# Kernel tuning notes

Measured on AMD Instinct MI355X. Metric: run time of the kernel, lower is better.

## Reference

```python
import jax, jax.numpy as jnp
import numpy as np

B, IN, H = 4096, 1024, 1024
G = 5  # i, f, o, c_hat, s gates

def setup_inputs() -> dict:
    key = jax.random.key(0)
    ks = jax.random.split(key, 24)
    s_in = 1.0 / np.sqrt(IN)
    s_h = 1.0 / np.sqrt(H)
    s_cat = 1.0 / np.sqrt(IN + H)
    inp = {
        'x': jax.random.normal(ks[0], (B, IN), jnp.float32),
        'h_prev': jax.random.normal(ks[1], (B, H), jnp.float32),
        'c_prev': jax.random.normal(ks[2], (B, H), jnp.float32),
        'ssg_state': jax.random.normal(ks[3], (B, H), jnp.float32),
        # stacked gate weights, torch Linear convention y = x @ W.T + b
        'Wx': jax.random.uniform(ks[4], (G, H, IN), jnp.float32, -s_in, s_in),
        'bWx': jax.random.uniform(ks[5], (G, H), jnp.float32, -s_in, s_in),
        'Ux': jax.random.uniform(ks[6], (G, H, H), jnp.float32, -s_h, s_h),
        'bUx': jax.random.uniform(ks[7], (G, H), jnp.float32, -s_h, s_h),
        # alpha MLP: Linear(IN+H -> H), ReLU, Linear(H -> 1), Sigmoid
        'a1_w': jax.random.uniform(ks[8], (H, IN + H), jnp.float32, -s_cat, s_cat),
        'a1_b': jax.random.uniform(ks[9], (H,), jnp.float32, -s_cat, s_cat),
        'a2_w': jax.random.uniform(ks[10], (1, H), jnp.float32, -s_h, s_h),
        'a2_b': jax.random.uniform(ks[11], (1,), jnp.float32, -s_h, s_h),
        'r1_w': jax.random.uniform(ks[12], (H, H), jnp.float32, -s_h, s_h),
        'r1_b': jax.random.uniform(ks[13], (H,), jnp.float32, -s_h, s_h),
        'r2_w': jax.random.uniform(ks[14], (H, H), jnp.float32, -s_h, s_h),
        'r2_b': jax.random.uniform(ks[15], (H,), jnp.float32, -s_h, s_h),
        'r3_w': jax.random.uniform(ks[16], (H, H), jnp.float32, -s_h, s_h),
        'r3_b': jax.random.uniform(ks[17], (H,), jnp.float32, -s_h, s_h),
        'ssg_w': jax.random.uniform(ks[18], (H, H), jnp.float32, -s_h, s_h),
        'ssg_b': jax.random.uniform(ks[19], (H,), jnp.float32, -s_h, s_h),
    }
    return inp


def reference(x, h_prev, c_prev, ssg_state, Wx, bWx, Ux, bUx,
              a1_w, a1_b, a2_w, a2_b, r1_w, r1_b, r2_w, r2_b, r3_w, r3_b,
              ssg_w, ssg_b):
    # all 5 gate pre-activations in two batched GEMMs: [G, B, H]
    g = (jnp.einsum('bi,ghi->gbh', x, Wx) + bWx[:, None, :]
         + jnp.einsum('bh,gkh->gbk', h_prev, Ux) + bUx[:, None, :])
    i_t = jax.nn.sigmoid(g[0])
    f_t = jax.nn.sigmoid(g[1])
    o_t = jax.nn.sigmoid(g[2])
    c_hat_t = jnp.tanh(g[3])
    s_t = jax.nn.sigmoid(g[4])  # computed as in original (unused when ssg_state given)

    combined = jnp.concatenate([x, h_prev], axis=-1)  # [B, IN+H]
    a_hidden = jax.nn.relu(combined @ a1_w.T + a1_b)
    alpha_t = jax.nn.sigmoid(a_hidden @ a2_w.T + a2_b)  # [B, 1]

    ssg_new = (ssg_state + h_prev) @ ssg_w.T + ssg_b  # ssg_state is not None branch

    c_t = f_t * c_prev + i_t * c_hat_t * s_t * alpha_t * ssg_new

    r = jax.nn.relu(h_prev @ r1_w.T + r1_b)
    r = jax.nn.relu(r @ r2_w.T + r2_b)
    residual = r @ r3_w.T + r3_b

    c_t = c_t + residual
    h_t = o_t * jnp.tanh(c_t)
    return (h_t, c_t, ssg_new)
```

## Files before the change

kernel.cpp:

```cpp
#include <hip/hip_runtime.h>
#include <hip/hip_bf16.h>

#define B_DIM 4096
#define H_DIM 1024
#define K1    2048
#define N1    6144

typedef __attribute__((ext_vector_type(8))) short bf16x8;
typedef __attribute__((ext_vector_type(4))) float f32x4;

__device__ __forceinline__ unsigned short f2bf(float f) {
  unsigned int x = __float_as_uint(f);
  x += 0x7fffu + ((x >> 16) & 1u);
  return (unsigned short)(x >> 16);
}
__device__ __forceinline__ float bf2f(unsigned short u) {
  return __uint_as_float(((unsigned int)u) << 16);
}
__device__ __forceinline__ float fast_sigmoid(float x) {
  return __builtin_amdgcn_rcpf(1.0f + __expf(-x));
}
__device__ __forceinline__ float fast_tanh(float x) {
  return 1.0f - 2.0f * __builtin_amdgcn_rcpf(1.0f + __expf(2.0f * x));
}
__device__ __forceinline__ void gload_lds16(const void* g, void* l) {
  __builtin_amdgcn_global_load_lds(
      (const __attribute__((address_space(1))) void*)g,
      (__attribute__((address_space(3))) void*)l, 16, 0, 0);
}

__device__ __forceinline__ int swz1k(int x) {
  return x ^ (((x >> 9) & 1) << 5);
}

__global__ __launch_bounds__(256) void prep_kernel(
    const float* __restrict__ x, const float* __restrict__ h,
    const float* __restrict__ ssg_state,
    const float* __restrict__ Wx, const float* __restrict__ Ux,
    const float* __restrict__ a1_w,
    const float* __restrict__ ssg_w, const float* __restrict__ r1_w,
    const float* __restrict__ r2_w, const float* __restrict__ r3_w,
    unsigned short* __restrict__ combined,
    unsigned short* __restrict__ ssg_in,
    unsigned short* __restrict__ W1,
    unsigned short* __restrict__ W2,
    unsigned short* __restrict__ W3,
    unsigned short* __restrict__ W4)
{
  const size_t NV0 = (size_t)B_DIM * K1 / 4;
  const size_t NV1 = (size_t)B_DIM * H_DIM / 4;
  const size_t NV3 = (size_t)N1 * K1 / 4;
  const size_t NV4 = (size_t)2048 * H_DIM / 4;
  const size_t NV5 = (size_t)H_DIM * H_DIM / 4;
  const size_t total = NV0 + NV1 + NV3 + NV4 + NV5 + NV5;
  const size_t stride = (size_t)gridDim.x * blockDim.x;

  for (size_t v = (size_t)blockIdx.x * blockDim.x + threadIdx.x; v < total; v += stride) {
    size_t idx = v;
    const float* src;
    unsigned short* dst;
    if (idx < NV0) {
      size_t e = idx * 4, b = e >> 11, k = e & 2047;
      src = (k < 1024) ? &x[(b << 10) + k] : &h[(b << 10) + (k - 1024)];
      dst = &combined[e];
    } else if ((idx -= NV0) < NV1) {
      size_t e = idx * 4;
      float4 a = *(const float4*)&ssg_state[e];
      float4 c = *(const float4*)&h[e];
      ushort4 o;
      o.x = f2bf(a.x + c.x); o.y = f2bf(a.y + c.y);
      o.z = f2bf(a.z + c.z); o.w = f2bf(a.w + c.w);
      *(ushort4*)&ssg_in[e] = o;
      continue;
    } else if ((idx -= NV1) < NV3) {
      size_t e = idx * 4, n = e >> 11, k = e & 2047;
      if (n < 5120) src = (k < 1024) ? &Wx[(n << 10) + k] : &Ux[(n << 10) + (k - 1024)];
      else          src = &a1_w[((n - 5120) << 11) + k];
      dst = &W1[e];
    } else if ((idx -= NV3) < NV4) {
      size_t e = idx * 4, n = e >> 10, k = e & 1023;
      src = (n < 1024) ? &ssg_w[(n << 10) + k] : &r1_w[((n - 1024) << 10) + k];
      dst = &W2[e];
    } else if ((idx -= NV4) < NV5) {
      size_t e = idx * 4; src = &r2_w[e]; dst = &W3[e];
    } else {
      idx -= NV5;
      size_t e = idx * 4; src = &r3_w[e]; dst = &W4[e];
    }
    float4 a = *(const float4*)src;
    ushort4 o;
    o.x = f2bf(a.x); o.y = f2bf(a.y); o.z = f2bf(a.z); o.w = f2bf(a.w);
    *(ushort4*)dst = o;
  }
}

template <int NT, int MODE>
__global__ __launch_bounds__(256, 2) void gemm_fr(
    const unsigned short* __restrict__ A0,
    const unsigned short* __restrict__ A1,
    const unsigned short* __restrict__ W,
    const float* __restrict__ b0, const float* __restrict__ b1,
    const float* __restrict__ b2,
    void* __restrict__ out0, void* __restrict__ out1)
{
  __shared__ unsigned short lds[32768];

  constexpr int KDIM = NT * 64;
  constexpr int N    = (MODE == 0) ? N1 : 2048;
  constexpr int NTN  = N / 128;
  constexpr int NWG  = (B_DIM / 128) * NTN;

  const int tid  = threadIdx.x;
  const int wave = tid >> 6;
  const int lane = tid & 63;
  const int wm = wave >> 1;
  const int wn = wave & 1;

  const int swz = (blockIdx.x & 7) * (NWG / 8) + (blockIdx.x >> 3);
  const int tm = swz / NTN, tn = swz % NTN;
  const int tmB = tm * 128, tnB = tn * 128;

  const unsigned short* Abase = A0;
  int lda = (MODE == 0) ? K1 : 1024;
  if (MODE == 1 && tn >= 8) { Abase = A1; lda = 2048; }

  const int sidx = swz1k(lane * 16);
  const int r_l  = sidx >> 6;
  const int kel  = (sidx & 63) >> 1;
  const unsigned short* pA[2][2];
  const unsigned short* pB[2][2];
#pragma unroll
  for (int rg = 0; rg < 2; ++rg)
#pragma unroll
    for (int j = 0; j < 2; ++j) {
      const int rr = wave * 32 + rg * 16 + r_l;
      const int kk0 = j * 32 + kel;
      pA[rg][j] = Abase + (size_t)(tmB + rr) * lda + kk0;
      pB[rg][j] = W + (size_t)(tnB + rr) * KDIM + kk0;
    }

#define STAGE_A(tt) do { const int p_ = (tt) & 1;                                \
    _Pragma("unroll")                                                            \
    for (int rg = 0; rg < 2; ++rg)                                               \
      _Pragma("unroll")                                                          \
      for (int j = 0; j < 2; ++j)                                                \
        gload_lds16(pA[rg][j] + (size_t)(tt) * 64,                               \
                    &lds[p_ * 16384 + ((wave * 2 + rg) * 2 + j) * 512]);         \
  } while (0)
#define STAGE_B(tt) do { const int p_ = (tt) & 1;                                \
    _Pragma("unroll")                                                            \
    for (int rg = 0; rg < 2; ++rg)                                               \
      _Pragma("unroll")                                                          \
      for (int j = 0; j < 2; ++j)                                                \
        gload_lds16(pB[rg][j] + (size_t)(tt) * 64,                               \
                    &lds[p_ * 16384 + 8192 + ((wave * 2 + rg) * 2 + j) * 512]);  \
  } while (0)

  const int loc = swz1k((lane & 15) * 64 + (lane >> 4) * 16);

  f32x4 acc[4][4];
#pragma unroll
  for (int m = 0; m < 4; ++m)
#pragma unroll
    for (int n = 0; n < 4; ++n) acc[m][n] = (f32x4){0.f, 0.f, 0.f, 0.f};

  STAGE_A(0); STAGE_B(0);

#define MFMA16(aV, bV) do {                                                      \
    _Pragma("unroll")                                                            \
    for (int n = 0; n < 4; ++n) {                                                \
      _Pragma("unroll")                                                          \
      for (int m = 0; m < 4; ++m)                                                \
        acc[m][n] = __builtin_amdgcn_mfma_f32_16x16x32_bf16(                     \
            aV[m], bV[n], acc[m][n], 0, 0, 0);                                   \
    } } while (0)

  const char* lchar = (const char*)lds;
  for (int t = 0; t < NT; ++t) {
    asm volatile("s_waitcnt vmcnt(0)" ::: "memory");
    __builtin_amdgcn_s_barrier();

    const char* base = lchar + (t & 1) * 32768;
    const char* bA = base + wm * 8192 + loc;
    const char* bB = base + 16384 + wn * 8192 + loc;

    bf16x8 a0[4], a1[4], b0[4], b1[4];
#pragma unroll
    for (int n = 0; n < 4; ++n) b0[n] = *(const bf16x8*)(bB + (2 * n + 0) * 1024);
#pragma unroll
    for (int m = 0; m < 4; ++m) a0[m] = *(const bf16x8*)(bA + (2 * m + 0) * 1024);
    if (t + 1 < NT) STAGE_A(t + 1);
#pragma unroll
    for (int n = 0; n < 4; ++n) b1[n] = *(const bf16x8*)(bB + (2 * n + 1) * 1024);
#pragma unroll
    for (int m = 0; m < 4; ++m) a1[m] = *(const bf16x8*)(bA + (2 * m + 1) * 1024);
    if (t + 1 < NT) STAGE_B(t + 1);

    __builtin_amdgcn_s_setprio(1);
    MFMA16(a0, b0);
    __builtin_amdgcn_s_setprio(0);
    __builtin_amdgcn_s_setprio(1);
    MFMA16(a1, b1);
    __builtin_amdgcn_s_setprio(0);
  }
#undef MFMA16
#undef STAGE_A
#undef STAGE_B

  const int l15 = lane & 15, lq4 = (lane >> 4) << 2;
  const int rowg0 = tmB + wm * 64;

  if (MODE == 1 && tn < 8) {
    const int col0 = tn * 128 + wn * 64;
#pragma unroll
    for (int fn = 0; fn < 4; ++fn) {
      const int col = col0 + fn * 16 + l15;
      const float bias = b0[col];
#pragma unroll
      for (int fm = 0; fm < 4; ++fm) {
        f32x4 v = acc[fm][fn];
#pragma unroll
        for (int j = 0; j < 4; ++j) {
          const int r = rowg0 + fm * 16 + lq4 + j;
          ((float*)out0)[(size_t)r * 1024 + col] = v[j] + bias;
        }
      }
    }
    return;
  }

  unsigned short* slab = &lds[wave * 1024];
  const int lr8 = lane >> 3, lc8 = lane & 7;
  bool isgate = false;
  int g = 0, colg0, rowplane = 0;
  unsigned short* outbase;
  if (MODE == 0) {
    isgate = (tn < 40);
    g = tn >> 3;
    colg0 = (isgate ? (tn & 7) : (tn - 40)) * 128 + wn * 64;
    outbase = isgate ? ((unsigned short*)out0 + (size_t)g * ((size_t)B_DIM * 1024))
                     : (unsigned short*)out1;
    (void)rowplane;
  } else {
    colg0 = (tn - 8) * 128 + wn * 64;
    outbase = (unsigned short*)out1;
  }
  float biasv[4];
#pragma unroll
  for (int fn = 0; fn < 4; ++fn) {
    const int c = colg0 + fn * 16 + l15;
    if (MODE == 0) biasv[fn] = isgate ? (b0[g * 1024 + c] + b1[g * 1024 + c]) : b2[c];
    else           biasv[fn] = b1[c];
  }
  __builtin_amdgcn_s_barrier();
#pragma unroll
  for (int fm = 0; fm < 4; ++fm) {
#pragma unroll
    for (int fn = 0; fn < 4; ++fn) {
      f32x4 v = acc[fm][fn];
#pragma unroll
      for (int j = 0; j < 4; ++j) {
        const int row = lq4 + j;
        const float xv = v[j] + biasv[fn];
        float res;
        if (MODE == 0 && isgate) res = (g == 3) ? fast_tanh(xv) : fast_sigmoid(xv);
        else                     res = fmaxf(xv, 0.f);
        const int colb = ((fn * 16 + l15) * 2) ^ (((row >> 2) & 3) << 5);
        slab[(row * 128 + colb) >> 1] = f2bf(res);
      }
    }
    asm volatile("s_waitcnt lgkmcnt(0)" ::: "memory");
    __builtin_amdgcn_sched_barrier(0);
#pragma unroll
    for (int rd = 0; rd < 2; ++rd) {
      const int row = rd * 8 + lr8;
      const int cb = (lc8 * 16) ^ (((row >> 2) & 3) << 5);
      bf16x8 pk = *(const bf16x8*)((const char*)slab + row * 128 + cb);
      const size_t r = (size_t)(rowg0 + fm * 16 + row);
      *(bf16x8*)&outbase[r * 1024 + colg0 + lc8 * 8] = pk;
    }
    asm volatile("s_waitcnt lgkmcnt(0)" ::: "memory");
    __builtin_amdgcn_sched_barrier(0);
  }
}

template <int MODE>
__global__ __launch_bounds__(256, 3) void gemm_bf16(
    const unsigned short* __restrict__ A0g,
    const unsigned short* __restrict__ Wg,
    const int M, const int N, const int K,
    const float* __restrict__ b0,
    void* __restrict__ out0)
{
  __shared__ unsigned short As[128 * 64];
  __shared__ unsigned short Bs[128 * 64];

  const int tid  = threadIdx.x;
  const int wave = tid >> 6;
  const int lane = tid & 63;
  const int wm = wave >> 1, wn = wave & 1;

  const int ntn = N >> 7;
  const int tm = blockIdx.x / ntn;
  const int tn = blockIdx.x % ntn;

  const int lrow = lane >> 3;
  const int lk   = (lane & 7) * 8;
  size_t a_off[4], b_off[4];
#pragma unroll
  for (int i = 0; i < 4; ++i) {
    int c = wave * 4 + i;
    int row = c * 8 + lrow;
    a_off[i] = (size_t)(tm * 128 + row) * K + lk;
    b_off[i] = (size_t)(tn * 128 + row) * K + lk;
  }

  f32x4 acc[4][4];
#pragma unroll
  for (int m = 0; m < 4; ++m)
#pragma unroll
    for (int n = 0; n < 4; ++n) acc[m][n] = (f32x4){0.f, 0.f, 0.f, 0.f};

  const int arow  = wm * 64 + (lane & 15);
  const int brow  = wn * 64 + (lane & 15);
  const int kfrag = (lane >> 4) * 8;

  for (int k0 = 0; k0 < K; k0 += 64) {
#pragma unroll
    for (int i = 0; i < 4; ++i) {
      gload_lds16(A0g + a_off[i] + k0, &As[(wave * 4 + i) * 512]);
      gload_lds16(Wg + b_off[i] + k0, &Bs[(wave * 4 + i) * 512]);
    }
    __syncthreads();
#pragma unroll
    for (int kk = 0; kk < 2; ++kk) {
      bf16x8 af[4], bfr[4];
#pragma unroll
      for (int m = 0; m < 4; ++m)
        af[m] = *(const bf16x8*)&As[(arow + m * 16) * 64 + kk * 32 + kfrag];
#pragma unroll
      for (int n = 0; n < 4; ++n)
        bfr[n] = *(const bf16x8*)&Bs[(brow + n * 16) * 64 + kk * 32 + kfrag];
#pragma unroll
      for (int m = 0; m < 4; ++m)
#pragma unroll
        for (int n = 0; n < 4; ++n)
          acc[m][n] = __builtin_amdgcn_mfma_f32_16x16x32_bf16(
              af[m], bfr[n], acc[m][n], 0, 0, 0);
    }
    __syncthreads();
  }

  const int col0 = tn * 128 + wn * 64;
  const int row0 = tm * 128 + wm * 64 + ((lane >> 4) << 2);
#pragma unroll
  for (int n = 0; n < 4; ++n) {
    const int col = col0 + n * 16 + (lane & 15);
    const float bias = b0[col];
#pragma unroll
    for (int m = 0; m < 4; ++m) {
      const int rowb = row0 + m * 16;
      f32x4 v = acc[m][n];
#pragma unroll
      for (int j = 0; j < 4; ++j) {
        const float xv = v[j] + bias;
        const int r = rowb + j;
        if (MODE == 2) {
          ((unsigned short*)out0)[(size_t)r * 1024 + col] = f2bf(fmaxf(xv, 0.f));
        } else {
          ((float*)out0)[(size_t)r * 1024 + col] = xv;
        }
      }
    }
  }
}

__global__ __launch_bounds__(256) void final_fused(
    const unsigned short* __restrict__ gates,
    const float* __restrict__ c_prev,
    const unsigned short* __restrict__ a_hidden,
    const float* __restrict__ a2_w, const float* __restrict__ a2_b,
    const float* __restrict__ residual,
    const float* __restrict__ ssg_new,
    float* __restrict__ h_out, float* __restrict__ c_out)
{
  __shared__ float red[5];
  const int r = blockIdx.x;
  const int tid = threadIdx.x;
  const size_t BH = (size_t)B_DIM * H_DIM;

  {
    ushort4 u = *(const ushort4*)&a_hidden[(size_t)r * 1024 + tid * 4];
    float4 w = *(const float4*)&a2_w[tid * 4];
    float s = bf2f(u.x) * w.x + bf2f(u.y) * w.y + bf2f(u.z) * w.z + bf2f(u.w) * w.w;
#pragma unroll
    for (int off = 32; off; off >>= 1) s += __shfl_xor(s, off);
    if ((tid & 63) == 0) red[tid >> 6] = s;
  }
  __syncthreads();
  if (tid == 0)
    red[4] = fast_sigmoid(red[0] + red[1] + red[2] + red[3] + a2_b[0]);
  __syncthreads();
  const float al = red[4];

  const size_t e = (size_t)r * 1024 + tid * 4;
  ushort4 iu = *(const ushort4*)&gates[e];
  ushort4 fu = *(const ushort4*)&gates[BH + e];
  ushort4 ou = *(const ushort4*)&gates[2 * BH + e];
  ushort4 cu = *(const ushort4*)&gates[3 * BH + e];
  ushort4 su = *(const ushort4*)&gates[4 * BH + e];
  float4 cp = *(const float4*)&c_prev[e];
  float4 rs = *(const float4*)&residual[e];
  float4 sg = *(const float4*)&ssg_new[e];
  float4 ho, co;
  co.x = bf2f(fu.x) * cp.x + bf2f(iu.x) * bf2f(cu.x) * bf2f(su.x) * al * sg.x + rs.x;
  co.y = bf2f(fu.y) * cp.y + bf2f(iu.y) * bf2f(cu.y) * bf2f(su.y) * al * sg.y + rs.y;
  co.z = bf2f(fu.z) * cp.z + bf2f(iu.z) * bf2f(cu.z) * bf2f(su.z) * al * sg.z + rs.z;
  co.w = bf2f(fu.w) * cp.w + bf2f(iu.w) * bf2f(cu.w) * bf2f(su.w) * al * sg.w + rs.w;
  ho.x = bf2f(ou.x) * fast_tanh(co.x);
  ho.y = bf2f(ou.y) * fast_tanh(co.y);
  ho.z = bf2f(ou.z) * fast_tanh(co.z);
  ho.w = bf2f(ou.w) * fast_tanh(co.w);
  *(float4*)&h_out[e] = ho;
  *(float4*)&c_out[e] = co;
}

extern "C" void kernel_launch(void* const* d_in, const int* in_sizes, int n_in,
                              void* d_out, int out_size, void* d_ws, size_t ws_size,
                              hipStream_t stream)
{
  (void)in_sizes; (void)n_in; (void)out_size; (void)ws_size;
  const float* x         = (const float*)d_in[0];
  const float* h_prev    = (const float*)d_in[1];
  const float* c_prev    = (const float*)d_in[2];
  const float* ssg_state = (const float*)d_in[3];
  const float* Wx        = (const float*)d_in[4];
  const float* bWx       = (const float*)d_in[5];
  const float* Ux        = (const float*)d_in[6];
  const float* bUx       = (const float*)d_in[7];
  const float* a1_w      = (const float*)d_in[8];
  const float* a1_b      = (const float*)d_in[9];
  const float* a2_w      = (const float*)d_in[10];
  const float* a2_b      = (const float*)d_in[11];
  const float* r1_w      = (const float*)d_in[12];
  const float* r1_b      = (const float*)d_in[13];
  const float* r2_w      = (const float*)d_in[14];
  const float* r2_b      = (const float*)d_in[15];
  const float* r3_w      = (const float*)d_in[16];
  const float* r3_b      = (const float*)d_in[17];
  const float* ssg_w     = (const float*)d_in[18];
  const float* ssg_b     = (const float*)d_in[19];

  char* ws = (char*)d_ws;
  unsigned short* combined = (unsigned short*)(ws);
  unsigned short* ssg_in   = (unsigned short*)(ws + 16777216);
  unsigned short* W1       = (unsigned short*)(ws + 33554432);
  unsigned short* W2       = (unsigned short*)(ws + 58720256);
  unsigned short* W3       = (unsigned short*)(ws + 62914560);
  unsigned short* W4       = (unsigned short*)(ws + 65011712);
  unsigned short* gates    = (unsigned short*)(ws + 67108864);
  unsigned short* a_hidden = (unsigned short*)(ws + 109051904);
  unsigned short* r1       = (unsigned short*)(ws + 117456896);
  unsigned short* r2       = (unsigned short*)(ws + 125845504);
  float*          residual = (float*)(ws + 134234112);

  float* h_out   = (float*)d_out;
  float* c_out   = h_out + (size_t)B_DIM * H_DIM;
  float* ssg_out = c_out + (size_t)B_DIM * H_DIM;

  prep_kernel<<<4096, 256, 0, stream>>>(x, h_prev, ssg_state, Wx, Ux, a1_w,
                                        ssg_w, r1_w, r2_w, r3_w,
                                        combined, ssg_in, W1, W2, W3, W4);

  gemm_fr<32, 0><<<(B_DIM / 128) * (N1 / 128), 256, 0, stream>>>(
      combined, nullptr, W1, bWx, bUx, a1_b, gates, a_hidden);

  gemm_fr<16, 1><<<(B_DIM / 128) * (2048 / 128), 256, 0, stream>>>(
      ssg_in, combined + 1024, W2, ssg_b, r1_b, nullptr, ssg_out, r1);

  gemm_bf16<2><<<(B_DIM / 128) * (1024 / 128), 256, 0, stream>>>(
      r1, W3, B_DIM, 1024, 1024, r2_b, r2);

  gemm_bf16<3><<<(B_DIM / 128) * (1024 / 128), 256, 0, stream>>>(
      r2, W4, B_DIM, 1024, 1024, r3_b, residual);

  final_fused<<<B_DIM, 256, 0, stream>>>(
      gates, c_prev, a_hidden, a2_w, a2_b, residual, ssg_out, h_out, c_out);
}
```

Measured before the change: 247.9 us.

## Merge the two large GEMM launches and reuse the pipelined GEMM body for residual layers

Turns the pipelined, double-buffered GEMM kernel into a device function. The gate/alpha GEMM and the ssg/r1 GEMM now run in a single launch that dispatches on block index, which removes the tail gap between the two kernels. The simpler gemm_bf16 used for the r2 and r3 layers is replaced by the same pipelined body, with new modes for bf16-ReLU output and fp32 output. The combined launch mixes two different K lengths in one grid, which may cause load imbalance, and the residual GEMMs lose their 3-blocks-per-CU occupancy hint.

```diff
diff --git a/kernel.cpp b/kernel.cpp
--- a/kernel.cpp
+++ b/kernel.cpp
@@ -95,7 +95,8 @@
 }
 
 template <int NT, int MODE>
-__global__ __launch_bounds__(256, 2) void gemm_fr(
+__device__ __forceinline__ void gemm_body(
+    unsigned short* lds, const int bid,
     const unsigned short* __restrict__ A0,
     const unsigned short* __restrict__ A1,
     const unsigned short* __restrict__ W,
@@ -103,12 +104,9 @@
     const float* __restrict__ b2,
     void* __restrict__ out0, void* __restrict__ out1)
 {
-  __shared__ unsigned short lds[32768];
-
   constexpr int KDIM = NT * 64;
-  constexpr int N    = (MODE == 0) ? N1 : 2048;
-  constexpr int NTN  = N / 128;
-  constexpr int NWG  = (B_DIM / 128) * NTN;
+  constexpr int NTN  = (MODE == 0) ? 48 : (MODE == 1 ? 16 : 8);
+  constexpr int NWG  = 32 * NTN;
 
   const int tid  = threadIdx.x;
   const int wave = tid >> 6;
@@ -116,7 +114,7 @@
   const int wm = wave >> 1;
   const int wn = wave & 1;
 
-  const int swz = (blockIdx.x & 7) * (NWG / 8) + (blockIdx.x >> 3);
+  const int swz = (bid & 7) * (NWG / 8) + (bid >> 3);
   const int tm = swz / NTN, tn = swz % NTN;
   const int tmB = tm * 128, tnB = tn * 128;
 
@@ -184,23 +182,23 @@
     const char* bA = base + wm * 8192 + loc;
     const char* bB = base + 16384 + wn * 8192 + loc;
 
-    bf16x8 a0[4], a1[4], b0[4], b1[4];
-#pragma unroll
-    for (int n = 0; n < 4; ++n) b0[n] = *(const bf16x8*)(bB + (2 * n + 0) * 1024);
+    bf16x8 a0[4], a1[4], b0v[4], b1v[4];
+#pragma unroll
+    for (int n = 0; n < 4; ++n) b0v[n] = *(const bf16x8*)(bB + (2 * n + 0) * 1024);
 #pragma unroll
     for (int m = 0; m < 4; ++m) a0[m] = *(const bf16x8*)(bA + (2 * m + 0) * 1024);
     if (t + 1 < NT) STAGE_A(t + 1);
 #pragma unroll
-    for (int n = 0; n < 4; ++n) b1[n] = *(const bf16x8*)(bB + (2 * n + 1) * 1024);
+    for (int n = 0; n < 4; ++n) b1v[n] = *(const bf16x8*)(bB + (2 * n + 1) * 1024);
 #pragma unroll
     for (int m = 0; m < 4; ++m) a1[m] = *(const bf16x8*)(bA + (2 * m + 1) * 1024);
     if (t + 1 < NT) STAGE_B(t + 1);
 
     __builtin_amdgcn_s_setprio(1);
-    MFMA16(a0, b0);
+    MFMA16(a0, b0v);
     __builtin_amdgcn_s_setprio(0);
     __builtin_amdgcn_s_setprio(1);
-    MFMA16(a1, b1);
+    MFMA16(a1, b1v);
     __builtin_amdgcn_s_setprio(0);
   }
 #undef MFMA16
@@ -210,7 +208,7 @@
   const int l15 = lane & 15, lq4 = (lane >> 4) << 2;
   const int rowg0 = tmB + wm * 64;
 
-  if (MODE == 1 && tn < 8) {
+  if ((MODE == 1 && tn < 8) || MODE == 3) {
     const int col0 = tn * 128 + wn * 64;
 #pragma unroll
     for (int fn = 0; fn < 4; ++fn) {
@@ -232,7 +230,7 @@
   unsigned short* slab = &lds[wave * 1024];
   const int lr8 = lane >> 3, lc8 = lane & 7;
   bool isgate = false;
-  int g = 0, colg0, rowplane = 0;
+  int g = 0, colg0;
   unsigned short* outbase;
   if (MODE == 0) {
     isgate = (tn < 40);
@@ -240,9 +238,11 @@
     colg0 = (isgate ? (tn & 7) : (tn - 40)) * 128 + wn * 64;
     outbase = isgate ? ((unsigned short*)out0 + (size_t)g * ((size_t)B_DIM * 1024))
                      : (unsigned short*)out1;
-    (void)rowplane;
+  } else if (MODE == 1) {
+    colg0 = (tn - 8) * 128 + wn * 64;
+    outbase = (unsigned short*)out1;
   } else {
-    colg0 = (tn - 8) * 128 + wn * 64;
+    colg0 = tn * 128 + wn * 64;
     outbase = (unsigned short*)out1;
   }
   float biasv[4];
@@ -284,95 +284,42 @@
   }
 }
 
+__global__ __launch_bounds__(256, 2) void gemm_big(
+    const unsigned short* __restrict__ combined,
+    const unsigned short* __restrict__ ssg_in,
+    const unsigned short* __restrict__ W1,
+    const unsigned short* __restrict__ W2,
+    const float* __restrict__ bWx, const float* __restrict__ bUx,
+    const float* __restrict__ a1_b,
+    const float* __restrict__ ssg_b, const float* __restrict__ r1_b,
+    unsigned short* __restrict__ gates,
+    unsigned short* __restrict__ a_hidden,
+    float* __restrict__ ssg_out,
+    unsigned short* __restrict__ r1)
+{
+  __shared__ unsigned short lds[32768];
+  const int bid = blockIdx.x;
+  if (bid < 1536) {
+    gemm_body<32, 0>(lds, bid, combined, nullptr, W1,
+                     bWx, bUx, a1_b, gates, a_hidden);
+  } else {
+    gemm_body<16, 1>(lds, bid - 1536, ssg_in, combined + 1024, W2,
+                     ssg_b, r1_b, nullptr, ssg_out, r1);
+  }
+}
+
 template <int MODE>
-__global__ __launch_bounds__(256, 3) void gemm_bf16(
-    const unsigned short* __restrict__ A0g,
-    const unsigned short* __restrict__ Wg,
-    const int M, const int N, const int K,
-    const float* __restrict__ b0,
-    void* __restrict__ out0)
-{
-  __shared__ unsigned short As[128 * 64];
-  __shared__ unsigned short Bs[128 * 64];
-
-  const int tid  = threadIdx.x;
-  const int wave = tid >> 6;
-  const int lane = tid & 63;
-  const int wm = wave >> 1, wn = wave & 1;
-
-  const int ntn = N >> 7;
-  const int tm = blockIdx.x / ntn;
-  const int tn = blockIdx.x % ntn;
-
-  const int lrow = lane >> 3;
-  const int lk   = (lane & 7) * 8;
-  size_t a_off[4], b_off[4];
-#pragma unroll
-  for (int i = 0; i < 4; ++i) {
-    int c = wave * 4 + i;
-    int row = c * 8 + lrow;
-    a_off[i] = (size_t)(tm * 128 + row) * K + lk;
-    b_off[i] = (size_t)(tn * 128 + row) * K + lk;
-  }
-
-  f32x4 acc[4][4];
-#pragma unroll
-  for (int m = 0; m < 4; ++m)
-#pragma unroll
-    for (int n = 0; n < 4; ++n) acc[m][n] = (f32x4){0.f, 0.f, 0.f, 0.f};
-
-  const int arow  = wm * 64 + (lane & 15);
-  const int brow  = wn * 64 + (lane & 15);
-  const int kfrag = (lane >> 4) * 8;
-
-  for (int k0 = 0; k0 < K; k0 += 64) {
-#pragma unroll
-    for (int i = 0; i < 4; ++i) {
-      gload_lds16(A0g + a_off[i] + k0, &As[(wave * 4 + i) * 512]);
-      gload_lds16(Wg + b_off[i] + k0, &Bs[(wave * 4 + i) * 512]);
-    }
-    __syncthreads();
-#pragma unroll
-    for (int kk = 0; kk < 2; ++kk) {
-      bf16x8 af[4], bfr[4];
-#pragma unroll
-      for (int m = 0; m < 4; ++m)
-        af[m] = *(const bf16x8*)&As[(arow + m * 16) * 64 + kk * 32 + kfrag];
-#pragma unroll
-      for (int n = 0; n < 4; ++n)
-        bfr[n] = *(const bf16x8*)&Bs[(brow + n * 16) * 64 + kk * 32 + kfrag];
-#pragma unroll
-      for (int m = 0; m < 4; ++m)
-#pragma unroll
-        for (int n = 0; n < 4; ++n)
-          acc[m][n] = __builtin_amdgcn_mfma_f32_16x16x32_bf16(
-              af[m], bfr[n], acc[m][n], 0, 0, 0);
-    }
-    __syncthreads();
-  }
-
-  const int col0 = tn * 128 + wn * 64;
-  const int row0 = tm * 128 + wm * 64 + ((lane >> 4) << 2);
-#pragma unroll
-  for (int n = 0; n < 4; ++n) {
-    const int col = col0 + n * 16 + (lane & 15);
-    const float bias = b0[col];
-#pragma unroll
-    for (int m = 0; m < 4; ++m) {
-      const int rowb = row0 + m * 16;
-      f32x4 v = acc[m][n];
-#pragma unroll
-      for (int j = 0; j < 4; ++j) {
-        const float xv = v[j] + bias;
-        const int r = rowb + j;
-        if (MODE == 2) {
-          ((unsigned short*)out0)[(size_t)r * 1024 + col] = f2bf(fmaxf(xv, 0.f));
-        } else {
-          ((float*)out0)[(size_t)r * 1024 + col] = xv;
-        }
-      }
-    }
-  }
+__global__ __launch_bounds__(256, 2) void gemm_small(
+    const unsigned short* __restrict__ A,
+    const unsigned short* __restrict__ W,
+    const float* __restrict__ bias,
+    void* __restrict__ out)
+{
+  __shared__ unsigned short lds[32768];
+  if (MODE == 2) gemm_body<16, 2>(lds, blockIdx.x, A, nullptr, W,
+                                  nullptr, bias, nullptr, nullptr, out);
+  else           gemm_body<16, 3>(lds, blockIdx.x, A, nullptr, W,
+                                  bias, nullptr, nullptr, out, nullptr);
 }
 
 __global__ __launch_bounds__(256) void final_fused(
@@ -472,17 +419,13 @@
                                         ssg_w, r1_w, r2_w, r3_w,
                                         combined, ssg_in, W1, W2, W3, W4);
 
-  gemm_fr<32, 0><<<(B_DIM / 128) * (N1 / 128), 256, 0, stream>>>(
-      combined, nullptr, W1, bWx, bUx, a1_b, gates, a_hidden);
-
-  gemm_fr<16, 1><<<(B_DIM / 128) * (2048 / 128), 256, 0, stream>>>(
-      ssg_in, combined + 1024, W2, ssg_b, r1_b, nullptr, ssg_out, r1);
-
-  gemm_bf16<2><<<(B_DIM / 128) * (1024 / 128), 256, 0, stream>>>(
-      r1, W3, B_DIM, 1024, 1024, r2_b, r2);
-
-  gemm_bf16<3><<<(B_DIM / 128) * (1024 / 128), 256, 0, stream>>>(
-      r2, W4, B_DIM, 1024, 1024, r3_b, residual);
+  gemm_big<<<2048, 256, 0, stream>>>(
+      combined, ssg_in, W1, W2, bWx, bUx, a1_b, ssg_b, r1_b,
+      gates, a_hidden, ssg_out, r1);
+
+  gemm_small<2><<<256, 256, 0, stream>>>(r1, W3, r2_b, r2);
+
+  gemm_small<3><<<256, 256, 0, stream>>>(r2, W4, r3_b, residual);
 
   final_fused<<<B_DIM, 256, 0, stream>>>(
       gates, c_prev, a_hidden, a2_w, a2_b, residual, ssg_out, h_out, c_out);
```

Result: faster. 224.0 us (-9.6%).
